# Performance work log

Hardware: AMD Instinct MI355X
Metric: run time of the kernel (lower is better)

Reference implementation:

```python
import jax, jax.numpy as jnp
import numpy as np

B, T, TS, J, D, H = 4, 512, 512, 17, 256, 8
CD = D // H
SCALE = CD ** -0.5


def setup_inputs() -> dict:
    key = jax.random.key(0)
    ks = jax.random.split(key, 7)
    return {
        "q": jax.random.normal(ks[0], (B, T, J, D), dtype=jnp.float32),
        "kv": jax.random.normal(ks[1], (B, TS, J, D), dtype=jnp.float32),
        "Wq": jax.random.normal(ks[2], (D, D), dtype=jnp.float32) * (D ** -0.5),
        "Wk": jax.random.normal(ks[3], (D, D), dtype=jnp.float32) * (D ** -0.5),
        "Wv": jax.random.normal(ks[4], (D, D), dtype=jnp.float32) * (D ** -0.5),
        "Wp": jax.random.normal(ks[5], (D, D), dtype=jnp.float32) * (D ** -0.5),
        "bp": jnp.zeros((D,), dtype=jnp.float32),
    }


def reference(q, kv, Wq, Wk, Wv, Wp, bp):
    b, t, j, d = q.shape
    t_sup = kv.shape[1]
    h, cd = H, CD
    # linear projections (torch Linear: x @ W^T), split heads -> [b,h,j,t,cd]
    qh = (q @ Wq.T).reshape(b, t, j, h, cd).transpose(0, 3, 2, 1, 4)
    kh = (kv @ Wk.T).reshape(b, t_sup, j, h, cd).transpose(0, 3, 2, 1, 4)
    vh = (kv @ Wv.T).reshape(b, t_sup, j, h, cd).transpose(0, 3, 2, 1, 4)
    # full attention matrix over temporal axes: [b,h,j,t,t_sup]
    scores = jnp.einsum("bhjtc,bhjsc->bhjts", qh, kh) * SCALE
    attn = jax.nn.softmax(scores, axis=-1)
    out = jnp.einsum("bhjts,bhjsc->bhjtc", attn, vh)
    out = out.transpose(0, 3, 2, 1, 4).reshape(b, t, j, d)  # [b,t,j,d]
    return out @ Wp.T + bp
```

## Files before the change

### kernel.cpp

```cpp
#include <hip/hip_runtime.h>
#include <hip/hip_bf16.h>

#define BB 4
#define TT 512
#define JJ 17
#define DD 256
#define HH 8
#define MROWS (BB*TT*JJ)
#define SZE ((size_t)MROWS * DD)
#define WSZ (DD*DD)
#define QSCALE 0.2550265247510319f
#define RST (17*256)

typedef short v8s __attribute__((ext_vector_type(8)));
typedef float v4f __attribute__((ext_vector_type(4)));

__device__ __forceinline__ unsigned short f2bf(float f) {
    union { float f; unsigned int u; } c; c.f = f;
    unsigned int u = c.u;
    return (unsigned short)((u + 0x7FFF + ((u >> 16) & 1)) >> 16);
}
__device__ __forceinline__ unsigned int pkbf(float lo, float hi) {
    union { float f; unsigned int u; } a, b; a.f = lo; b.f = hi;
    return __builtin_amdgcn_perm(b.u + 0x8000u, a.u + 0x8000u, 0x07060302u);
}
__device__ __forceinline__ float fexp2(float x) {
    return __builtin_amdgcn_exp2f(x);
}

__device__ __forceinline__ void gld16(const unsigned short* g, unsigned short* l) {
    __builtin_amdgcn_global_load_lds(
        (const __attribute__((address_space(1))) void*)g,
        (__attribute__((address_space(3))) void*)l,
        16, 0, 0);
}

__global__ __launch_bounds__(256) void prep_kernel(
    const float* __restrict__ q, const float* __restrict__ kv,
    const float* __restrict__ Wq, const float* __restrict__ Wk,
    const float* __restrict__ Wv, const float* __restrict__ Wp,
    unsigned short* __restrict__ qb, unsigned short* __restrict__ kvb,
    unsigned short* __restrict__ Wqb, unsigned short* __restrict__ Wkb,
    unsigned short* __restrict__ Wvb, unsigned short* __restrict__ Wpb)
{
    size_t i = ((size_t)blockIdx.x * 256 + threadIdx.x) * 8;
    const float* src; unsigned short* dst; size_t off; float scale = 1.f;
    if (i < SZE)            { src = q;  dst = qb;  off = i;        scale = QSCALE; }
    else if (i < 2 * SZE)   { src = kv; dst = kvb; off = i - SZE; }
    else {
        size_t k = i - 2 * SZE;
        int w = (int)(k >> 16);
        off = k & (WSZ - 1);
        src = (w == 0) ? Wq : (w == 1) ? Wk : (w == 2) ? Wv : Wp;
        dst = (w == 0) ? Wqb : (w == 1) ? Wkb : (w == 2) ? Wvb : Wpb;
    }
    float4 x0 = *(const float4*)(src + off);
    float4 x1 = *(const float4*)(src + off + 4);
    union { unsigned short s[8]; int4 v; } u;
    u.s[0] = f2bf(x0.x * scale); u.s[1] = f2bf(x0.y * scale);
    u.s[2] = f2bf(x0.z * scale); u.s[3] = f2bf(x0.w * scale);
    u.s[4] = f2bf(x1.x * scale); u.s[5] = f2bf(x1.y * scale);
    u.s[6] = f2bf(x1.z * scale); u.s[7] = f2bf(x1.w * scale);
    *(int4*)(dst + off) = u.v;
}

__global__ __launch_bounds__(512) void gemm_kernel(
    const unsigned short* __restrict__ A0,
    const unsigned short* __restrict__ A1,
    const unsigned short* __restrict__ A2,
    const unsigned short* __restrict__ W0,
    const unsigned short* __restrict__ W1,
    const unsigned short* __restrict__ W2,
    unsigned short* __restrict__ Y0,
    unsigned short* __restrict__ Y1,
    unsigned short* __restrict__ Y2,
    const float* __restrict__ bias,
    float* __restrict__ outf,
    int fp32out)
{
    const int z = blockIdx.y;
    const unsigned short* A = (z == 0) ? A0 : (z == 1) ? A1 : A2;
    const unsigned short* W = (z == 0) ? W0 : (z == 1) ? W1 : W2;
    unsigned short* Y       = (z == 0) ? Y0 : (z == 1) ? Y1 : Y2;

    const int bm = blockIdx.x;

    __shared__ unsigned short As[2][128 * 32];
    __shared__ unsigned short Bs[2][256 * 32];

    const int tid  = threadIdx.x;
    const int wv   = tid >> 6;
    const int lane = tid & 63;
    const int wm   = wv & 1;
    const int wn   = wv >> 1;
    const int quad = lane >> 4;
    const int l16  = lane & 15;

    const int s     = lane >> 2;
    const int chunk = lane & 3;
    const int fsw   = (s ^ (s >> 2)) & 3;
    const int cg    = chunk ^ fsw;
    const int srow  = wv * 16 + s;
    const unsigned short* gA  = A + (size_t)(bm * 128 + srow) * 256 + cg * 8;
    const unsigned short* gB0 = W + (size_t)srow * 256 + cg * 8;
    const unsigned short* gB1 = W + (size_t)(128 + srow) * 256 + cg * 8;
    unsigned short* lA  = &As[0][wv * 512 + lane * 8];
    unsigned short* lB0 = &Bs[0][wv * 512 + lane * 8];
    unsigned short* lB1 = &Bs[0][4096 + wv * 512 + lane * 8];

    const int rch8 = (quad ^ ((l16 ^ (l16 >> 2)) & 3)) * 8;

    v4f acc[4][4] = {};

    gld16(gA,  lA);
    gld16(gB0, lB0);
    gld16(gB1, lB1);
    __syncthreads();

    for (int kt = 0; kt < 8; ++kt) {
        const int cur = kt & 1;
        if (kt < 7) {
            const int nk = (kt + 1) * 32;
            const int nb = cur ^ 1;
            gld16(gA  + nk, lA  + nb * 4096);
            gld16(gB0 + nk, lB0 + nb * 8192);
            gld16(gB1 + nk, lB1 + nb * 8192);
        }
        v8s a[4], b[4];
        #pragma unroll
        for (int i = 0; i < 4; ++i)
            a[i] = *(const v8s*)(&As[cur][(wm * 64 + i * 16 + l16) * 32 + rch8]);
        #pragma unroll
        for (int j = 0; j < 4; ++j)
            b[j] = *(const v8s*)(&Bs[cur][(wn * 64 + j * 16 + l16) * 32 + rch8]);
        #pragma unroll
        for (int i = 0; i < 4; ++i)
            #pragma unroll
            for (int j = 0; j < 4; ++j)
                acc[i][j] = __builtin_amdgcn_mfma_f32_16x16x32_bf16(
                    a[i], b[j], acc[i][j], 0, 0, 0);
        __syncthreads();
    }

    #pragma unroll
    for (int i = 0; i < 4; ++i) {
        #pragma unroll
        for (int j = 0; j < 4; ++j) {
            #pragma unroll
            for (int r = 0; r < 4; ++r) {
                int gm = bm * 128 + wm * 64 + i * 16 + quad * 4 + r;
                int gn = wn * 64 + j * 16 + l16;
                float v = acc[i][j][r];
                if (fp32out)
                    outf[(size_t)gm * 256 + gn] = v + bias[gn];
                else
                    Y[(size_t)gm * 256 + gn] = f2bf(v);
            }
        }
    }
}

#define VST 136
#define PST 72

__global__ __launch_bounds__(256) void attn_kernel(
    const unsigned short* __restrict__ Qp,
    const unsigned short* __restrict__ Kp,
    const unsigned short* __restrict__ Vp,
    unsigned short* __restrict__ Att)
{
    const int bjh = blockIdx.x;
    const int qt  = blockIdx.y;
    const int h   = bjh & 7;
    const int bj  = bjh >> 3;
    const int j   = bj % 17;
    const int b_  = bj / 17;

    __shared__ unsigned short Ks[128 * 40];
    __shared__ unsigned short Vs[32 * VST];
    __shared__ unsigned short Ps[128 * PST];
    __shared__ float Ls[128];

    const int tid  = threadIdx.x;
    const int wave = tid >> 6;
    const int lane = tid & 63;
    const int quad = lane >> 4;
    const int l16  = lane & 15;

    const int base0 = b_ * 512 * RST + j * 256 + h * 32;

    v8s qa[2];
    #pragma unroll
    for (int fi = 0; fi < 2; ++fi)
        qa[fi] = *(const v8s*)(
            Qp + base0 + (qt * 128 + wave * 32 + fi * 16 + l16) * RST + quad * 8);

    float lacc[2] = {0.f, 0.f};
    v4f accO[2][2] = {};

    for (int kc = 0; kc < 4; ++kc) {
        __syncthreads();
        #pragma unroll
        for (int c = 0; c < 2; ++c) {
            int krow = wave * 16 + l16 + c * 64;
            *(int4*)(&Ks[krow * 40 + quad * 8]) = *(const int4*)(
                Kp + base0 + (kc * 128 + krow) * RST + quad * 8);
        }
        #pragma unroll
        for (int c = 0; c < 2; ++c) {
            int idx  = c * 256 + tid;
            int srow = idx >> 2;
            int cd0  = (idx & 3) << 3;
            int xof  = (((srow >> 3) ^ (cd0 >> 3)) << 3) + (srow & 7);
            union { int4 v; unsigned short s[8]; } u;
            u.v = *(const int4*)(
                Vp + base0 + (kc * 128 + srow) * RST + cd0);
            #pragma unroll
            for (int i = 0; i < 8; ++i)
                Vs[(cd0 + i) * VST + xof] = u.s[i];
        }
        __syncthreads();

        #pragma unroll
        for (int half = 0; half < 2; ++half) {
            v4f accST[4][2] = {};
            __builtin_amdgcn_s_setprio(1);
            #pragma unroll
            for (int si = 0; si < 4; ++si) {
                v8s kb = *(const v8s*)(&Ks[((half * 4 + si) * 16 + l16) * 40 + quad * 8]);
                #pragma unroll
                for (int fi = 0; fi < 2; ++fi)
                    accST[si][fi] = __builtin_amdgcn_mfma_f32_16x16x32_bf16(
                        kb, qa[fi], accST[si][fi], 0, 0, 0);
            }
            __builtin_amdgcn_s_setprio(0);
            #pragma unroll
            for (int fi = 0; fi < 2; ++fi) {
                int prow = (wave * 32 + fi * 16 + l16) * PST;
                #pragma unroll
                for (int si = 0; si < 4; ++si) {
                    float p0 = fexp2(accST[si][fi][0]);
                    float p1 = fexp2(accST[si][fi][1]);
                    float p2 = fexp2(accST[si][fi][2]);
                    float p3 = fexp2(accST[si][fi][3]);
                    lacc[fi] += (p0 + p1) + (p2 + p3);
                    uint2 pk;
                    pk.x = pkbf(p0, p1);
                    pk.y = pkbf(p2, p3);
                    *(uint2*)(&Ps[prow + si * 16 + quad * 4]) = pk;
                }
            }
            asm volatile("s_waitcnt lgkmcnt(0)" ::: "memory");

            __builtin_amdgcn_s_setprio(1);
            #pragma unroll
            for (int ks = 0; ks < 2; ++ks) {
                v8s pa[2];
                #pragma unroll
                for (int fi = 0; fi < 2; ++fi)
                    pa[fi] = *(const v8s*)(&Ps[(wave * 32 + fi * 16 + l16) * PST +
                                               ks * 32 + quad * 8]);
                #pragma unroll
                for (int nj = 0; nj < 2; ++nj) {
                    int cd  = nj * 16 + l16;
                    int blk = (half * 8 + ks * 4 + quad) ^ (cd >> 3);
                    v8s vb = *(const v8s*)(&Vs[cd * VST + (blk << 3)]);
                    #pragma unroll
                    for (int fi = 0; fi < 2; ++fi)
                        accO[fi][nj] = __builtin_amdgcn_mfma_f32_16x16x32_bf16(
                            pa[fi], vb, accO[fi][nj], 0, 0, 0);
                }
            }
            __builtin_amdgcn_s_setprio(0);
        }
    }

    #pragma unroll
    for (int fi = 0; fi < 2; ++fi) {
        float lv = lacc[fi];
        lv += __shfl_xor(lv, 16);
        lv += __shfl_xor(lv, 32);
        if (quad == 0) Ls[wave * 32 + fi * 16 + l16] = lv;
    }
    asm volatile("s_waitcnt lgkmcnt(0)" ::: "memory");

    #pragma unroll
    for (int fi = 0; fi < 2; ++fi) {
        float4 lv = *(float4*)(&Ls[wave * 32 + fi * 16 + quad * 4]);
        float rl[4] = {1.f / lv.x, 1.f / lv.y, 1.f / lv.z, 1.f / lv.w};
        #pragma unroll
        for (int nj = 0; nj < 2; ++nj) {
            #pragma unroll
            for (int r = 0; r < 4; ++r) {
                int trow = qt * 128 + wave * 32 + fi * 16 + quad * 4 + r;
                int cd   = nj * 16 + l16;
                float v  = accO[fi][nj][r] * rl[r];
                Att[(size_t)(base0 + trow * RST + cd)] = f2bf(v);
            }
        }
    }
}

extern "C" void kernel_launch(void* const* d_in, const int* in_sizes, int n_in,
                              void* d_out, int out_size, void* d_ws, size_t ws_size,
                              hipStream_t stream) {
    const float* q  = (const float*)d_in[0];
    const float* kv = (const float*)d_in[1];
    const float* Wq = (const float*)d_in[2];
    const float* Wk = (const float*)d_in[3];
    const float* Wv = (const float*)d_in[4];
    const float* Wp = (const float*)d_in[5];
    const float* bp = (const float*)d_in[6];

    unsigned short* ws  = (unsigned short*)d_ws;
    unsigned short* Qp  = ws;
    unsigned short* Kp  = ws + SZE;
    unsigned short* Vp  = ws + 2 * SZE;
    unsigned short* qb  = ws + 3 * SZE;
    unsigned short* kvb = ws + 4 * SZE;
    unsigned short* Wqb = ws + 5 * SZE;
    unsigned short* Wkb = Wqb + WSZ;
    unsigned short* Wvb = Wkb + WSZ;
    unsigned short* Wpb = Wvb + WSZ;
    unsigned short* Att = qb;
    float* out = (float*)d_out;

    prep_kernel<<<8832, 256, 0, stream>>>(q, kv, Wq, Wk, Wv, Wp,
                                          qb, kvb, Wqb, Wkb, Wvb, Wpb);
    gemm_kernel<<<dim3(272, 3), 512, 0, stream>>>(
        qb, kvb, kvb, Wqb, Wkb, Wvb, Qp, Kp, Vp, nullptr, nullptr, 0);
    attn_kernel<<<dim3(544, 4, 1), 256, 0, stream>>>(Qp, Kp, Vp, Att);
    gemm_kernel<<<dim3(272, 1), 512, 0, stream>>>(
        Att, Att, Att, Wpb, Wpb, Wpb, nullptr, nullptr, nullptr, bp, out, 1);
}
```

Before: 214.5 us.

## Prefetch K/V into registers in attention, add dedicated smaller output-projection GEMM

```diff
diff --git a/kernel.cpp b/kernel.cpp
--- a/kernel.cpp
+++ b/kernel.cpp
@@ -73,10 +73,7 @@
     const unsigned short* __restrict__ W2,
     unsigned short* __restrict__ Y0,
     unsigned short* __restrict__ Y1,
-    unsigned short* __restrict__ Y2,
-    const float* __restrict__ bias,
-    float* __restrict__ outf,
-    int fp32out)
+    unsigned short* __restrict__ Y2)
 {
     const int z = blockIdx.y;
     const unsigned short* A = (z == 0) ? A0 : (z == 1) ? A1 : A2;
@@ -143,34 +140,102 @@
     }
 
     #pragma unroll
-    for (int i = 0; i < 4; ++i) {
-        #pragma unroll
-        for (int j = 0; j < 4; ++j) {
+    for (int i = 0; i < 4; ++i)
+        #pragma unroll
+        for (int j = 0; j < 4; ++j)
             #pragma unroll
             for (int r = 0; r < 4; ++r) {
                 int gm = bm * 128 + wm * 64 + i * 16 + quad * 4 + r;
                 int gn = wn * 64 + j * 16 + l16;
-                float v = acc[i][j][r];
-                if (fp32out)
-                    outf[(size_t)gm * 256 + gn] = v + bias[gn];
-                else
-                    Y[(size_t)gm * 256 + gn] = f2bf(v);
-            }
-        }
-    }
+                Y[(size_t)gm * 256 + gn] = f2bf(acc[i][j][r]);
+            }
+}
+
+__global__ __launch_bounds__(256) void gemmo_kernel(
+    const unsigned short* __restrict__ A,
+    const unsigned short* __restrict__ W,
+    const float* __restrict__ bias,
+    float* __restrict__ out)
+{
+    const int bm = blockIdx.x;
+
+    __shared__ unsigned short As[2][64 * 32];
+    __shared__ unsigned short Bs[2][256 * 32];
+
+    const int tid  = threadIdx.x;
+    const int lane = tid & 63;
+    const int wn   = tid >> 6;
+    const int quad = lane >> 4;
+    const int l16  = lane & 15;
+
+    const int arow  = tid >> 2;
+    const int chunk = tid & 3;
+    const int cgA   = (chunk ^ ((arow ^ (arow >> 2)) & 3)) * 8;
+    const unsigned short* gA = A + (size_t)(bm * 64 + arow) * 256 + cgA;
+    const unsigned short* gB = W + (size_t)arow * 256 + cgA;
+    unsigned short* lA = &As[0][tid * 8];
+    unsigned short* lB = &Bs[0][tid * 8];
+
+    const int rch8 = (quad ^ ((l16 ^ (l16 >> 2)) & 3)) * 8;
+
+    v4f acc[4][4] = {};
+
+    gld16(gA, lA);
+    #pragma unroll
+    for (int p = 0; p < 4; ++p)
+        gld16(gB + (size_t)p * 64 * 256, lB + p * 2048);
+    __syncthreads();
+
+    for (int kt = 0; kt < 8; ++kt) {
+        const int cur = kt & 1;
+        if (kt < 7) {
+            const int nk = (kt + 1) * 32;
+            const int nb = cur ^ 1;
+            gld16(gA + nk, lA + nb * 2048);
+            #pragma unroll
+            for (int p = 0; p < 4; ++p)
+                gld16(gB + (size_t)p * 64 * 256 + nk, lB + nb * 8192 + p * 2048);
+        }
+        v8s a[4], b[4];
+        #pragma unroll
+        for (int i = 0; i < 4; ++i)
+            a[i] = *(const v8s*)(&As[cur][(i * 16 + l16) * 32 + rch8]);
+        #pragma unroll
+        for (int j = 0; j < 4; ++j)
+            b[j] = *(const v8s*)(&Bs[cur][(wn * 64 + j * 16 + l16) * 32 + rch8]);
+        #pragma unroll
+        for (int i = 0; i < 4; ++i)
+            #pragma unroll
+            for (int j = 0; j < 4; ++j)
+                acc[i][j] = __builtin_amdgcn_mfma_f32_16x16x32_bf16(
+                    a[i], b[j], acc[i][j], 0, 0, 0);
+        __syncthreads();
+    }
+
+    #pragma unroll
+    for (int i = 0; i < 4; ++i)
+        #pragma unroll
+        for (int j = 0; j < 4; ++j)
+            #pragma unroll
+            for (int r = 0; r < 4; ++r) {
+                int gm = bm * 64 + i * 16 + quad * 4 + r;
+                int gn = wn * 64 + j * 16 + l16;
+                out[(size_t)gm * 256 + gn] = acc[i][j][r] + bias[gn];
+            }
 }
 
 #define VST 136
 #define PST 72
 
-__global__ __launch_bounds__(256) void attn_kernel(
+__global__ __launch_bounds__(256, 4) void attn_kernel(
     const unsigned short* __restrict__ Qp,
     const unsigned short* __restrict__ Kp,
     const unsigned short* __restrict__ Vp,
     unsigned short* __restrict__ Att)
 {
-    const int bjh = blockIdx.x;
-    const int qt  = blockIdx.y;
+    const int id  = blockIdx.x;
+    const int bjh = (id & 7) | ((id >> 5) << 3);
+    const int qt  = (id >> 3) & 3;
     const int h   = bjh & 7;
     const int bj  = bjh >> 3;
     const int j   = bj % 17;
@@ -195,31 +260,47 @@
         qa[fi] = *(const v8s*)(
             Qp + base0 + (qt * 128 + wave * 32 + fi * 16 + l16) * RST + quad * 8);
 
+    const int krow0 = wave * 16 + l16;
+    const int vsrow = tid >> 2;
+    const int vw    = tid & 3;
+    const int vcd0  = vw << 3;
+
     float lacc[2] = {0.f, 0.f};
     v4f accO[2][2] = {};
 
+    int4 kreg[2], vreg[2];
+    #pragma unroll
+    for (int c = 0; c < 2; ++c) {
+        kreg[c] = *(const int4*)(Kp + base0 + (krow0 + c * 64) * RST + quad * 8);
+        vreg[c] = *(const int4*)(Vp + base0 + (vsrow + c * 64) * RST + vcd0);
+    }
+
     for (int kc = 0; kc < 4; ++kc) {
+        #pragma unroll
+        for (int c = 0; c < 2; ++c)
+            *(int4*)(&Ks[(krow0 + c * 64) * 40 + quad * 8]) = kreg[c];
+        #pragma unroll
+        for (int c = 0; c < 2; ++c) {
+            int srow = vsrow + c * 64;
+            int xof  = (((srow >> 3) ^ vw) << 3) + (srow & 7);
+            union { int4 v; unsigned short s[8]; } u;
+            u.v = vreg[c];
+            #pragma unroll
+            for (int i = 0; i < 8; ++i) {
+                int m = (i + 2 * vw) & 7;
+                Vs[(vcd0 + m) * VST + xof] = u.s[m];
+            }
+        }
         __syncthreads();
-        #pragma unroll
-        for (int c = 0; c < 2; ++c) {
-            int krow = wave * 16 + l16 + c * 64;
-            *(int4*)(&Ks[krow * 40 + quad * 8]) = *(const int4*)(
-                Kp + base0 + (kc * 128 + krow) * RST + quad * 8);
-        }
-        #pragma unroll
-        for (int c = 0; c < 2; ++c) {
-            int idx  = c * 256 + tid;
-            int srow = idx >> 2;
-            int cd0  = (idx & 3) << 3;
-            int xof  = (((srow >> 3) ^ (cd0 >> 3)) << 3) + (srow & 7);
-            union { int4 v; unsigned short s[8]; } u;
-            u.v = *(const int4*)(
-                Vp + base0 + (kc * 128 + srow) * RST + cd0);
-            #pragma unroll
-            for (int i = 0; i < 8; ++i)
-                Vs[(cd0 + i) * VST + xof] = u.s[i];
-        }
-        __syncthreads();
+
+        if (kc < 3) {
+            const int nko = (kc + 1) * 128 * RST;
+            #pragma unroll
+            for (int c = 0; c < 2; ++c) {
+                kreg[c] = *(const int4*)(Kp + base0 + nko + (krow0 + c * 64) * RST + quad * 8);
+                vreg[c] = *(const int4*)(Vp + base0 + nko + (vsrow + c * 64) * RST + vcd0);
+            }
+        }
 
         #pragma unroll
         for (int half = 0; half < 2; ++half) {
@@ -273,6 +354,7 @@
             }
             __builtin_amdgcn_s_setprio(0);
         }
+        __syncthreads();
     }
 
     #pragma unroll
@@ -328,8 +410,7 @@
     prep_kernel<<<8832, 256, 0, stream>>>(q, kv, Wq, Wk, Wv, Wp,
                                           qb, kvb, Wqb, Wkb, Wvb, Wpb);
     gemm_kernel<<<dim3(272, 3), 512, 0, stream>>>(
-        qb, kvb, kvb, Wqb, Wkb, Wvb, Qp, Kp, Vp, nullptr, nullptr, 0);
-    attn_kernel<<<dim3(544, 4, 1), 256, 0, stream>>>(Qp, Kp, Vp, Att);
-    gemm_kernel<<<dim3(272, 1), 512, 0, stream>>>(
-        Att, Att, Att, Wpb, Wpb, Wpb, nullptr, nullptr, nullptr, bp, out, 1);
-}
+        qb, kvb, kvb, Wqb, Wkb, Wvb, Qp, Kp, Vp);
+    attn_kernel<<<dim3(2176), 256, 0, stream>>>(Qp, Kp, Vp, Att);
+    gemmo_kernel<<<dim3(544), 256, 0, stream>>>(Att, Wpb, bp, out);
+}
```

After: 253.4 us. 18.2% more time.
